# Optimization experiments

Measured on AMD Instinct MI355X. Metric: run time of the kernel, lower is better.

## Reference

```python
import jax, jax.numpy as jnp
import numpy as np

N = 50000
E = 1600000
IN, OUT = 128, 64


def _gcn(h, W, b, src, dst):
    # DGL GraphConv, norm='both', weight applied first (in>out), activation=relu
    x = h @ W  # [N, OUT]
    ones = jnp.ones((src.shape[0],), dtype=h.dtype)
    deg_out = jnp.clip(jax.ops.segment_sum(ones, src, num_segments=N), 1.0)
    deg_in = jnp.clip(jax.ops.segment_sum(ones, dst, num_segments=N), 1.0)
    x = x * jax.lax.rsqrt(deg_out)[:, None]
    agg = jax.ops.segment_sum(x[src], dst, num_segments=N)  # SpMM
    agg = agg * jax.lax.rsqrt(deg_in)[:, None]
    return jax.nn.relu(agg + b)


def setup_inputs() -> dict:
    key = jax.random.key(0)
    ks = jax.random.split(key, 10)
    inp = {"h": jax.random.normal(ks[0], (N, IN), dtype=jnp.float32)}
    for i in range(3):
        inp[f"src{i}"] = jax.random.randint(ks[1 + 2 * i], (E,), 0, N, dtype=jnp.int32)
        inp[f"dst{i}"] = jax.random.randint(ks[2 + 2 * i], (E,), 0, N, dtype=jnp.int32)
        inp[f"W{i}"] = jax.random.normal(ks[7 + i], (IN, OUT), dtype=jnp.float32) * (1.0 / np.sqrt(IN))
        inp[f"b{i}"] = jnp.zeros((OUT,), dtype=jnp.float32)
    return inp


def reference(h, src0, dst0, src1, dst1, src2, dst2, W0, b0, W1, b1, W2, b2):
    e0 = _gcn(h, W0, b0, src0, dst0)
    e1 = _gcn(h, W1, b1, src1, dst1)
    e2 = _gcn(h, W2, b2, src2, dst2)
    # stack over meta-path dim then mean == average of semantic embeddings
    return (e0 + e1 + e2) / 3.0
```

## Files before the change

kernel.cpp:

```cpp
#include <hip/hip_runtime.h>

#define KDIM 128
#define NCOLS 64
#define NHCH 64
#define HW 12500
#define BUCKET 64
#define NB7 782
#define FCAP 2816
#define NPB 85
#define PREP_HIST (3 * NHCH)
#define PREP_CNT  (3 * NPB)
#define PREP_WF   12
#define PREP_CONV 565
#define PREP_GRID (PREP_HIST + PREP_CNT + PREP_WF + PREP_CONV)

typedef __attribute__((ext_vector_type(8))) short bf16x8;
typedef __attribute__((ext_vector_type(4))) float f32x4;

struct GArgs {
  const int*   src[3];
  const int*   dst[3];
  const float* W[3];
  const float* b[3];
  int          E[3];
};

__device__ __forceinline__ unsigned short f2bf(float f) {
  unsigned u = __float_as_uint(f);
  u += 0x7FFFu + ((u >> 16) & 1u);
  return (unsigned short)(u >> 16);
}
__device__ __forceinline__ float bflo(unsigned u) { return __uint_as_float(u << 16); }
__device__ __forceinline__ float bfhi(unsigned u) { return __uint_as_float(u & 0xFFFF0000u); }

__global__ __launch_bounds__(256) void prep_kernel(
    GArgs A, const float* __restrict__ h, unsigned short* __restrict__ hb,
    unsigned short* __restrict__ Wf, unsigned* __restrict__ P8,
    int* __restrict__ tot, int total8) {
  __shared__ unsigned sbuf[HW];
  const int b = blockIdx.x;
  const int t = threadIdx.x;

  if (b < PREP_HIST) {
    const int g = b >> 6;
    const int chunk = b & 63;
    const int E = A.E[g];
    const int per_chunk = (((E + NHCH - 1) / NHCH) + 3) & ~3;
    const int* __restrict__ keys = A.src[g];
    for (int i = t; i < HW; i += 256) sbuf[i] = 0;
    __syncthreads();
    const int e0 = chunk * per_chunk;
    const int e1 = min(e0 + per_chunk, E);
    const int nn = max(e1 - e0, 0);
    const int nv = nn >> 2;
    const int4* k4p = (const int4*)&keys[e0];
    for (int v = t; v < nv; v += 256) {
      int4 k = k4p[v];
      atomicAdd(&sbuf[(unsigned)k.x >> 2], 1u << (((unsigned)k.x & 3u) * 8));
      atomicAdd(&sbuf[(unsigned)k.y >> 2], 1u << (((unsigned)k.y & 3u) * 8));
      atomicAdd(&sbuf[(unsigned)k.z >> 2], 1u << (((unsigned)k.z & 3u) * 8));
      atomicAdd(&sbuf[(unsigned)k.w >> 2], 1u << (((unsigned)k.w & 3u) * 8));
    }
    for (int e = e0 + (nv << 2) + t; e < e1; e += 256) {
      unsigned k = (unsigned)keys[e];
      atomicAdd(&sbuf[k >> 2], 1u << ((k & 3u) * 8));
    }
    __syncthreads();
    unsigned* __restrict__ dstp = P8 + (size_t)b * HW;
    for (int i = t; i < HW; i += 256) dstp[i] = sbuf[i];

  } else if (b < PREP_HIST + PREP_CNT) {
    const int bb = b - PREP_HIST;
    const int g = bb / NPB;
    const int blk = bb % NPB;
    const int E = A.E[g];
    const int per_block = (((E + NPB - 1) / NPB) + 3) & ~3;
    const int* __restrict__ dst = A.dst[g];
    int* hcnt = (int*)sbuf;
    for (int i = t; i < NB7; i += 256) hcnt[i] = 0;
    __syncthreads();
    const int e0 = blk * per_block;
    const int e1 = min(e0 + per_block, E);
    const int nn = max(e1 - e0, 0);
    const int nv = nn >> 2;
    const int4* d4 = (const int4*)&dst[e0];
    for (int v = t; v < nv; v += 256) {
      int4 d = d4[v];
      atomicAdd(&hcnt[(unsigned)d.x >> 6], 1);
      atomicAdd(&hcnt[(unsigned)d.y >> 6], 1);
      atomicAdd(&hcnt[(unsigned)d.z >> 6], 1);
      atomicAdd(&hcnt[(unsigned)d.w >> 6], 1);
    }
    for (int e = e0 + (nv << 2) + t; e < e1; e += 256)
      atomicAdd(&hcnt[(unsigned)dst[e] >> 6], 1);
    __syncthreads();
    for (int i = t; i < NB7; i += 256)
      if (hcnt[i]) atomicAdd(&tot[g * NB7 + i], hcnt[i]);

  } else if (b < PREP_HIST + PREP_CNT + PREP_WF) {
    int tid = (b - PREP_HIST - PREP_CNT) * 256 + t;
    int lane = tid & 63;
    int frag = (tid >> 6) & 15;
    int g = tid >> 10;
    int c = frag >> 2, kk = frag & 3;
    int n = lane & 15, quad = lane >> 4;
    const float* W = A.W[g];
    unsigned short v[8];
    #pragma unroll
    for (int j = 0; j < 8; ++j) {
      int k = 32 * kk + quad * 8 + j;
      v[j] = f2bf(W[k * 64 + 4 * n + c]);
    }
    uint4 u;
    u.x = (unsigned)v[0] | ((unsigned)v[1] << 16);
    u.y = (unsigned)v[2] | ((unsigned)v[3] << 16);
    u.z = (unsigned)v[4] | ((unsigned)v[5] << 16);
    u.w = (unsigned)v[6] | ((unsigned)v[7] << 16);
    ((uint4*)Wf)[tid] = u;

  } else {
    const int cb = b - (PREP_HIST + PREP_CNT + PREP_WF);
    for (int i = cb * 256 + t; i < total8; i += PREP_CONV * 256) {
      const float4* hp = (const float4*)(h + (size_t)i * 8);
      float4 f0 = hp[0];
      float4 f1 = hp[1];
      uint4 u;
      u.x = (unsigned)f2bf(f0.x) | ((unsigned)f2bf(f0.y) << 16);
      u.y = (unsigned)f2bf(f0.z) | ((unsigned)f2bf(f0.w) << 16);
      u.z = (unsigned)f2bf(f1.x) | ((unsigned)f2bf(f1.y) << 16);
      u.w = (unsigned)f2bf(f1.z) | ((unsigned)f2bf(f1.w) << 16);
      ((uint4*)hb)[i] = u;
    }
  }
}

__global__ __launch_bounds__(512) void scan782_kernel(
    const int* __restrict__ tot, int* __restrict__ off, int* __restrict__ cursor) {
  __shared__ int sd[512];
  const int g = blockIdx.x;
  const int t = threadIdx.x;
  int base = 0;
  for (int c0 = 0; c0 < NB7; c0 += 512) {
    int idx = c0 + t;
    int v = (idx < NB7) ? tot[g * NB7 + idx] : 0;
    sd[t] = v;
    __syncthreads();
    for (int o = 1; o < 512; o <<= 1) {
      int add = (t >= o) ? sd[t - o] : 0;
      __syncthreads();
      sd[t] += add;
      __syncthreads();
    }
    int excl = base + sd[t] - v;
    if (idx < NB7) {
      off[g * (NB7 + 1) + idx] = excl;
      cursor[g * NB7 + idx] = excl;
    }
    base += sd[511];
    __syncthreads();
  }
  if (t == 0) off[g * (NB7 + 1) + NB7] = base;
}

__global__ __launch_bounds__(256) void partition_fine_kernel(
    GArgs A, int* __restrict__ cursor, unsigned* __restrict__ P2, int Emax) {
  __shared__ int lcnt[NB7];
  __shared__ int lcur[NB7];
  const int g = blockIdx.y;
  const int E = A.E[g];
  const int per_block = (((E + NPB - 1) / NPB) + 3) & ~3;
  const int* __restrict__ src = A.src[g];
  const int* __restrict__ dst = A.dst[g];
  unsigned* __restrict__ P2g = P2 + (size_t)g * Emax;
  const int t = threadIdx.x;
  for (int i = t; i < NB7; i += 256) lcnt[i] = 0;
  __syncthreads();
  const int e0 = blockIdx.x * per_block;
  const int e1 = min(e0 + per_block, E);
  const int n = max(e1 - e0, 0);
  const int nv = n >> 2;
  const int4* d4 = (const int4*)&dst[e0];
  const int4* s4 = (const int4*)&src[e0];
  for (int v = t; v < nv; v += 256) {
    int4 d = d4[v];
    atomicAdd(&lcnt[(unsigned)d.x >> 6], 1);
    atomicAdd(&lcnt[(unsigned)d.y >> 6], 1);
    atomicAdd(&lcnt[(unsigned)d.z >> 6], 1);
    atomicAdd(&lcnt[(unsigned)d.w >> 6], 1);
  }
  for (int e = e0 + (nv << 2) + t; e < e1; e += 256)
    atomicAdd(&lcnt[(unsigned)dst[e] >> 6], 1);
  __syncthreads();
  for (int i = t; i < NB7; i += 256) {
    int c = lcnt[i];
    lcur[i] = c ? atomicAdd(&cursor[g * NB7 + i], c) : 0;
  }
  __syncthreads();
  for (int v = t; v < nv; v += 256) {
    int4 d = d4[v];
    int4 s = s4[v];
    unsigned bk; int pos;
    bk = (unsigned)d.x >> 6; pos = atomicAdd(&lcur[bk], 1);
    P2g[pos] = (unsigned)s.x | (((unsigned)d.x & 63u) << 16);
    bk = (unsigned)d.y >> 6; pos = atomicAdd(&lcur[bk], 1);
    P2g[pos] = (unsigned)s.y | (((unsigned)d.y & 63u) << 16);
    bk = (unsigned)d.z >> 6; pos = atomicAdd(&lcur[bk], 1);
    P2g[pos] = (unsigned)s.z | (((unsigned)d.z & 63u) << 16);
    bk = (unsigned)d.w >> 6; pos = atomicAdd(&lcur[bk], 1);
    P2g[pos] = (unsigned)s.w | (((unsigned)d.w & 63u) << 16);
  }
  for (int e = e0 + (nv << 2) + t; e < e1; e += 256) {
    unsigned d = (unsigned)dst[e];
    unsigned bk = d >> 6;
    int pos = atomicAdd(&lcur[bk], 1);
    P2g[pos] = (unsigned)src[e] | ((d & 63u) << 16);
  }
}

__global__ __launch_bounds__(512) void gemm_mfma_kernel(
    GArgs A, const unsigned short* __restrict__ hb,
    const unsigned short* __restrict__ Wf, const unsigned* __restrict__ P8,
    unsigned short* __restrict__ x, int N) {
  __shared__ unsigned ldegw[64];
  const int g = blockIdx.y;
  unsigned short* __restrict__ xg = x + (size_t)g * N * NCOLS;
  const int t = threadIdx.x;
  const int row0 = blockIdx.x * 128;

  if (t < 64) ldegw[t] = 0;
  __syncthreads();
  if (t < 256) {
    const unsigned* __restrict__ Pg = P8 + (size_t)g * NHCH * HW;
    const int widx = t >> 3;
    const int cg = t & 7;
    const int wcol = min((row0 >> 2) + widx, HW - 1);
    unsigned lo = 0, hi = 0;
    #pragma unroll
    for (int cc = 0; cc < 8; ++cc) {
      unsigned wv = Pg[(size_t)(cg * 8 + cc) * HW + wcol];
      lo += wv & 0x00FF00FFu;
      hi += (wv >> 8) & 0x00FF00FFu;
    }
    atomicAdd(&ldegw[2 * widx], lo);
    atomicAdd(&ldegw[2 * widx + 1], hi);
  }

  const int lane = t & 63;
  const int w = t >> 6;
  const int quad = lane >> 4;
  const int n = lane & 15;

  int arow = min(row0 + w * 16 + n, N - 1);
  const unsigned short* hrow = hb + (size_t)arow * KDIM + quad * 8;
  bf16x8 a0 = *(const bf16x8*)(hrow);
  bf16x8 a1 = *(const bf16x8*)(hrow + 32);
  bf16x8 a2 = *(const bf16x8*)(hrow + 64);
  bf16x8 a3 = *(const bf16x8*)(hrow + 96);

  const uint4* wfp = (const uint4*)Wf + (size_t)g * 1024 + lane;

  f32x4 acc[4];
  #pragma unroll
  for (int c = 0; c < 4; ++c) acc[c] = (f32x4)(0.f);

  __syncthreads();

  #pragma unroll
  for (int c = 0; c < 4; ++c) {
    union { uint4 u; bf16x8 v; } b0, b1, b2, b3;
    b0.u = wfp[(size_t)(c * 4 + 0) * 64];
    b1.u = wfp[(size_t)(c * 4 + 1) * 64];
    b2.u = wfp[(size_t)(c * 4 + 2) * 64];
    b3.u = wfp[(size_t)(c * 4 + 3) * 64];
    acc[c] = __builtin_amdgcn_mfma_f32_16x16x32_bf16(a0, b0.v, acc[c], 0, 0, 0);
    acc[c] = __builtin_amdgcn_mfma_f32_16x16x32_bf16(a1, b1.v, acc[c], 0, 0, 0);
    acc[c] = __builtin_amdgcn_mfma_f32_16x16x32_bf16(a2, b2.v, acc[c], 0, 0, 0);
    acc[c] = __builtin_amdgcn_mfma_f32_16x16x32_bf16(a3, b3.v, acc[c], 0, 0, 0);
  }

  const int rbase = row0 + w * 16 + quad * 4;
  #pragma unroll
  for (int r = 0; r < 4; ++r) {
    int row = rbase + r;
    if (row < N) {
      int lr = row - row0;
      float dg = (float)((ldegw[2 * (lr >> 2) + (lr & 1)] >> (((lr >> 1) & 1) * 16)) & 0xFFFFu);
      float s = rsqrtf(fmaxf(dg, 1.0f));
      uint2 o;
      o.x = (unsigned)f2bf(acc[0][r] * s) | ((unsigned)f2bf(acc[1][r] * s) << 16);
      o.y = (unsigned)f2bf(acc[2][r] * s) | ((unsigned)f2bf(acc[3][r] * s) << 16);
      *(uint2*)(xg + (size_t)row * NCOLS + 4 * n) = o;
    }
  }
}

__global__ __launch_bounds__(512) void spmm_all_kernel(
    GArgs A, const unsigned* __restrict__ P2, const int* __restrict__ off,
    const unsigned short* __restrict__ x, float* __restrict__ out,
    int N, int Emax) {
  __shared__ unsigned eb[FCAP];
  __shared__ unsigned short srcs[FCAP];
  __shared__ int cnt[BUCKET];
  __shared__ int cur[BUCKET];
  __shared__ int rsx[BUCKET + 1];

  const int t = threadIdx.x;
  const int bk = blockIdx.x;
  const int dbase = bk * BUCKET;
  const int nd = min(BUCKET, N - dbase);
  const int grp = t >> 3;
  const int qe = (t & 7) * 8;

  float tot[8];
  #pragma unroll
  for (int j = 0; j < 8; ++j) tot[j] = 0.f;

  for (int g = 0; g < 3; ++g) {
    const unsigned* __restrict__ P2g = P2 + (size_t)g * Emax;
    const unsigned short* __restrict__ xg = x + (size_t)g * N * NCOLS;

    __syncthreads();
    if (t < BUCKET) cnt[t] = 0;
    __syncthreads();

    const int e0 = off[g * (NB7 + 1) + bk];
    const int ne = min(off[g * (NB7 + 1) + bk + 1] - e0, FCAP);
    for (int i = t; i < ne; i += 512) {
      unsigned e = P2g[e0 + i];
      eb[i] = e;
      atomicAdd(&cnt[e >> 16], 1);
    }
    __syncthreads();

    if (t < BUCKET) {
      int v = cnt[t];
      int incl = v;
      #pragma unroll
      for (int o = 1; o < 64; o <<= 1) {
        int u = __shfl_up(incl, o, 64);
        if (t >= o) incl += u;
      }
      rsx[t + 1] = incl;
      cur[t] = incl - v;
      if (t == 0) rsx[0] = 0;
    }
    __syncthreads();

    for (int i = t; i < ne; i += 512) {
      unsigned e = eb[i];
      int pos = atomicAdd(&cur[e >> 16], 1);
      srcs[pos] = (unsigned short)(e & 0xFFFFu);
    }
    __syncthreads();

    if (grp < nd) {
      int i = rsx[grp];
      const int iend = rsx[grp + 1];
      const int deg = iend - i;
      float acc[8];
      #pragma unroll
      for (int j = 0; j < 8; ++j) acc[j] = 0.f;
      for (; i + 3 < iend; i += 4) {
        int sa = srcs[i + 0];
        int sb = srcs[i + 1];
        int sc = srcs[i + 2];
        int sdd = srcs[i + 3];
        uint4 ua = *(const uint4*)&xg[(size_t)sa * NCOLS + qe];
        uint4 ub = *(const uint4*)&xg[(size_t)sb * NCOLS + qe];
        uint4 uc = *(const uint4*)&xg[(size_t)sc * NCOLS + qe];
        uint4 ud = *(const uint4*)&xg[(size_t)sdd * NCOLS + qe];
        acc[0] += bflo(ua.x) + bflo(ub.x) + bflo(uc.x) + bflo(ud.x);
        acc[1] += bfhi(ua.x) + bfhi(ub.x) + bfhi(uc.x) + bfhi(ud.x);
        acc[2] += bflo(ua.y) + bflo(ub.y) + bflo(uc.y) + bflo(ud.y);
        acc[3] += bfhi(ua.y) + bfhi(ub.y) + bfhi(uc.y) + bfhi(ud.y);
        acc[4] += bflo(ua.z) + bflo(ub.z) + bflo(uc.z) + bflo(ud.z);
        acc[5] += bfhi(ua.z) + bfhi(ub.z) + bfhi(uc.z) + bfhi(ud.z);
        acc[6] += bflo(ua.w) + bflo(ub.w) + bflo(uc.w) + bflo(ud.w);
        acc[7] += bfhi(ua.w) + bfhi(ub.w) + bfhi(uc.w) + bfhi(ud.w);
      }
      for (; i < iend; ++i) {
        int s = srcs[i];
        uint4 u = *(const uint4*)&xg[(size_t)s * NCOLS + qe];
        acc[0] += bflo(u.x); acc[1] += bfhi(u.x);
        acc[2] += bflo(u.y); acc[3] += bfhi(u.y);
        acc[4] += bflo(u.z); acc[5] += bfhi(u.z);
        acc[6] += bflo(u.w); acc[7] += bfhi(u.w);
      }
      float sc2 = rsqrtf(fmaxf((float)deg, 1.0f));
      const float* bg = A.b[g] + qe;
      #pragma unroll
      for (int j = 0; j < 8; ++j)
        tot[j] += fmaxf(fmaf(acc[j], sc2, bg[j]), 0.f) * (1.0f / 3.0f);
    }
  }

  if (grp < nd) {
    float* op = &out[(size_t)(dbase + grp) * NCOLS + qe];
    *(float4*)&op[0] = make_float4(tot[0], tot[1], tot[2], tot[3]);
    *(float4*)&op[4] = make_float4(tot[4], tot[5], tot[6], tot[7]);
  }
}

extern "C" void kernel_launch(void* const* d_in, const int* in_sizes, int n_in,
                              void* d_out, int out_size, void* d_ws, size_t ws_size,
                              hipStream_t stream) {
  const float* h = (const float*)d_in[0];
  const int N = in_sizes[0] / KDIM;
  float* out = (float*)d_out;

  GArgs A;
  int Emax = 0;
  for (int g = 0; g < 3; ++g) {
    A.src[g] = (const int*)  d_in[1 + g * 4];
    A.dst[g] = (const int*)  d_in[2 + g * 4];
    A.W[g]   = (const float*)d_in[3 + g * 4];
    A.b[g]   = (const float*)d_in[4 + g * 4];
    A.E[g]   = in_sizes[1 + g * 4];
    if (A.E[g] > Emax) Emax = A.E[g];
  }

  char* w = (char*)d_ws;
  unsigned short* x = (unsigned short*)w;
  char* w2 = w + (size_t)3 * N * NCOLS * sizeof(unsigned short);
  unsigned short* hb = (unsigned short*)w2;
  char* w3 = w2 + (size_t)N * KDIM * sizeof(unsigned short);
  unsigned* P2 = (unsigned*)w3;
  char* w4 = w3 + (size_t)3 * Emax * sizeof(unsigned);
  unsigned* P8 = (unsigned*)w4;
  char* w5 = w4 + (size_t)3 * NHCH * HW * sizeof(unsigned);
  unsigned short* Wf = (unsigned short*)w5;
  char* w6 = w5 + (size_t)3 * 16 * 64 * 8 * sizeof(unsigned short);
  int* tot    = (int*)w6;
  int* cursor = tot + 3 * NB7;
  int* off    = cursor + 3 * NB7;

  hipMemsetAsync(tot, 0, 3 * NB7 * sizeof(int), stream);
  const int total8 = N * KDIM / 8;
  prep_kernel<<<PREP_GRID, 256, 0, stream>>>(A, h, hb, Wf, P8, tot, total8);
  scan782_kernel<<<3, 512, 0, stream>>>(tot, off, cursor);
  partition_fine_kernel<<<dim3(NPB, 3), 256, 0, stream>>>(A, cursor, P2, Emax);
  gemm_mfma_kernel<<<dim3((N + 127) / 128, 3), 512, 0, stream>>>(A, hb, Wf, P8, x, N);
  spmm_all_kernel<<<NB7, 512, 0, stream>>>(A, P2, off, x, out, N, Emax);
}
```

Before: 263.9 us.

## Fuse scan, partition and GEMM into one heterogeneous kernel launch

Merges the bucket-offset scan, the fine partition and the MFMA GEMM into a single kernel whose blocks split by index into partition blocks and GEMM blocks. Each partition block redundantly scans the bucket totals itself, with block 0 writing the offsets. Its cursor now starts at zero, is memset along with the totals, and only accumulates a relative offset on top of the scan. This removes two kernel launches and their dependency gaps and lets partitioning overlap with the GEMM. In exchange each partition block repeats the scan, partition blocks now use 512 threads, and the GEMM blocks carry the partition's larger shared-memory footprint, which may reduce occupancy.

```diff
diff --git a/kernel.cpp b/kernel.cpp
--- a/kernel.cpp
+++ b/kernel.cpp
@@ -13,6 +13,10 @@
 #define PREP_WF   12
 #define PREP_CONV 565
 #define PREP_GRID (PREP_HIST + PREP_CNT + PREP_WF + PREP_CONV)
+#define PG_PART (3 * NPB)
+#define PG_GEMM_PER 391
+#define PG_GEMM (3 * PG_GEMM_PER)
+#define PG_GRID (PG_PART + PG_GEMM)
 
 typedef __attribute__((ext_vector_type(8))) short bf16x8;
 typedef __attribute__((ext_vector_type(4))) float f32x4;
@@ -134,162 +138,166 @@
   }
 }
 
-__global__ __launch_bounds__(512) void scan782_kernel(
-    const int* __restrict__ tot, int* __restrict__ off, int* __restrict__ cursor) {
-  __shared__ int sd[512];
-  const int g = blockIdx.x;
-  const int t = threadIdx.x;
-  int base = 0;
-  for (int c0 = 0; c0 < NB7; c0 += 512) {
-    int idx = c0 + t;
-    int v = (idx < NB7) ? tot[g * NB7 + idx] : 0;
-    sd[t] = v;
-    __syncthreads();
-    for (int o = 1; o < 512; o <<= 1) {
-      int add = (t >= o) ? sd[t - o] : 0;
-      __syncthreads();
-      sd[t] += add;
-      __syncthreads();
-    }
-    int excl = base + sd[t] - v;
-    if (idx < NB7) {
-      off[g * (NB7 + 1) + idx] = excl;
-      cursor[g * NB7 + idx] = excl;
-    }
-    base += sd[511];
-    __syncthreads();
-  }
-  if (t == 0) off[g * (NB7 + 1) + NB7] = base;
-}
-
-__global__ __launch_bounds__(256) void partition_fine_kernel(
-    GArgs A, int* __restrict__ cursor, unsigned* __restrict__ P2, int Emax) {
+__global__ __launch_bounds__(512) void pg_kernel(
+    GArgs A, const unsigned short* __restrict__ hb,
+    const unsigned short* __restrict__ Wf, const unsigned* __restrict__ P8,
+    const int* __restrict__ tot, int* __restrict__ cursor,
+    int* __restrict__ off, unsigned* __restrict__ P2,
+    unsigned short* __restrict__ x, int N, int Emax) {
   __shared__ int lcnt[NB7];
   __shared__ int lcur[NB7];
-  const int g = blockIdx.y;
-  const int E = A.E[g];
-  const int per_block = (((E + NPB - 1) / NPB) + 3) & ~3;
-  const int* __restrict__ src = A.src[g];
-  const int* __restrict__ dst = A.dst[g];
-  unsigned* __restrict__ P2g = P2 + (size_t)g * Emax;
+  __shared__ int sd[512];
+  const int b = blockIdx.x;
   const int t = threadIdx.x;
-  for (int i = t; i < NB7; i += 256) lcnt[i] = 0;
-  __syncthreads();
-  const int e0 = blockIdx.x * per_block;
-  const int e1 = min(e0 + per_block, E);
-  const int n = max(e1 - e0, 0);
-  const int nv = n >> 2;
-  const int4* d4 = (const int4*)&dst[e0];
-  const int4* s4 = (const int4*)&src[e0];
-  for (int v = t; v < nv; v += 256) {
-    int4 d = d4[v];
-    atomicAdd(&lcnt[(unsigned)d.x >> 6], 1);
-    atomicAdd(&lcnt[(unsigned)d.y >> 6], 1);
-    atomicAdd(&lcnt[(unsigned)d.z >> 6], 1);
-    atomicAdd(&lcnt[(unsigned)d.w >> 6], 1);
-  }
-  for (int e = e0 + (nv << 2) + t; e < e1; e += 256)
-    atomicAdd(&lcnt[(unsigned)dst[e] >> 6], 1);
-  __syncthreads();
-  for (int i = t; i < NB7; i += 256) {
-    int c = lcnt[i];
-    lcur[i] = c ? atomicAdd(&cursor[g * NB7 + i], c) : 0;
-  }
-  __syncthreads();
-  for (int v = t; v < nv; v += 256) {
-    int4 d = d4[v];
-    int4 s = s4[v];
-    unsigned bk; int pos;
-    bk = (unsigned)d.x >> 6; pos = atomicAdd(&lcur[bk], 1);
-    P2g[pos] = (unsigned)s.x | (((unsigned)d.x & 63u) << 16);
-    bk = (unsigned)d.y >> 6; pos = atomicAdd(&lcur[bk], 1);
-    P2g[pos] = (unsigned)s.y | (((unsigned)d.y & 63u) << 16);
-    bk = (unsigned)d.z >> 6; pos = atomicAdd(&lcur[bk], 1);
-    P2g[pos] = (unsigned)s.z | (((unsigned)d.z & 63u) << 16);
-    bk = (unsigned)d.w >> 6; pos = atomicAdd(&lcur[bk], 1);
-    P2g[pos] = (unsigned)s.w | (((unsigned)d.w & 63u) << 16);
-  }
-  for (int e = e0 + (nv << 2) + t; e < e1; e += 256) {
-    unsigned d = (unsigned)dst[e];
-    unsigned bk = d >> 6;
-    int pos = atomicAdd(&lcur[bk], 1);
-    P2g[pos] = (unsigned)src[e] | ((d & 63u) << 16);
-  }
-}
-
-__global__ __launch_bounds__(512) void gemm_mfma_kernel(
-    GArgs A, const unsigned short* __restrict__ hb,
-    const unsigned short* __restrict__ Wf, const unsigned* __restrict__ P8,
-    unsigned short* __restrict__ x, int N) {
-  __shared__ unsigned ldegw[64];
-  const int g = blockIdx.y;
-  unsigned short* __restrict__ xg = x + (size_t)g * N * NCOLS;
-  const int t = threadIdx.x;
-  const int row0 = blockIdx.x * 128;
-
-  if (t < 64) ldegw[t] = 0;
-  __syncthreads();
-  if (t < 256) {
-    const unsigned* __restrict__ Pg = P8 + (size_t)g * NHCH * HW;
-    const int widx = t >> 3;
-    const int cg = t & 7;
-    const int wcol = min((row0 >> 2) + widx, HW - 1);
-    unsigned lo = 0, hi = 0;
+
+  if (b < PG_PART) {
+    const int g = b / NPB;
+    const int blk = b % NPB;
+    const int E = A.E[g];
+    const int per_block = (((E + NPB - 1) / NPB) + 3) & ~3;
+    const int* __restrict__ src = A.src[g];
+    const int* __restrict__ dst = A.dst[g];
+    unsigned* __restrict__ P2g = P2 + (size_t)g * Emax;
+
+    for (int i = t; i < NB7; i += 512) lcnt[i] = 0;
+    __syncthreads();
+    const int e0 = blk * per_block;
+    const int e1 = min(e0 + per_block, E);
+    const int nn = max(e1 - e0, 0);
+    const int nv = nn >> 2;
+    const int4* d4 = (const int4*)&dst[e0];
+    const int4* s4 = (const int4*)&src[e0];
+    for (int v = t; v < nv; v += 512) {
+      int4 d = d4[v];
+      atomicAdd(&lcnt[(unsigned)d.x >> 6], 1);
+      atomicAdd(&lcnt[(unsigned)d.y >> 6], 1);
+      atomicAdd(&lcnt[(unsigned)d.z >> 6], 1);
+      atomicAdd(&lcnt[(unsigned)d.w >> 6], 1);
+    }
+    for (int e = e0 + (nv << 2) + t; e < e1; e += 512)
+      atomicAdd(&lcnt[(unsigned)dst[e] >> 6], 1);
+    __syncthreads();
+
+    int base = 0;
+    for (int c0 = 0; c0 < NB7; c0 += 512) {
+      int idx = c0 + t;
+      int v = (idx < NB7) ? tot[g * NB7 + idx] : 0;
+      sd[t] = v;
+      __syncthreads();
+      for (int o = 1; o < 512; o <<= 1) {
+        int add = (t >= o) ? sd[t - o] : 0;
+        __syncthreads();
+        sd[t] += add;
+        __syncthreads();
+      }
+      int excl = base + sd[t] - v;
+      if (idx < NB7) {
+        lcur[idx] = excl;
+        if (blk == 0) off[g * (NB7 + 1) + idx] = excl;
+      }
+      base += sd[511];
+      __syncthreads();
+    }
+    if (blk == 0 && t == 0) off[g * (NB7 + 1) + NB7] = base;
+
+    for (int i = t; i < NB7; i += 512) {
+      int c = lcnt[i];
+      if (c) lcur[i] += atomicAdd(&cursor[g * NB7 + i], c);
+    }
+    __syncthreads();
+
+    for (int v = t; v < nv; v += 512) {
+      int4 d = d4[v];
+      int4 s = s4[v];
+      unsigned bk; int pos;
+      bk = (unsigned)d.x >> 6; pos = atomicAdd(&lcur[bk], 1);
+      P2g[pos] = (unsigned)s.x | (((unsigned)d.x & 63u) << 16);
+      bk = (unsigned)d.y >> 6; pos = atomicAdd(&lcur[bk], 1);
+      P2g[pos] = (unsigned)s.y | (((unsigned)d.y & 63u) << 16);
+      bk = (unsigned)d.z >> 6; pos = atomicAdd(&lcur[bk], 1);
+      P2g[pos] = (unsigned)s.z | (((unsigned)d.z & 63u) << 16);
+      bk = (unsigned)d.w >> 6; pos = atomicAdd(&lcur[bk], 1);
+      P2g[pos] = (unsigned)s.w | (((unsigned)d.w & 63u) << 16);
+    }
+    for (int e = e0 + (nv << 2) + t; e < e1; e += 512) {
+      unsigned d = (unsigned)dst[e];
+      unsigned bk = d >> 6;
+      int pos = atomicAdd(&lcur[bk], 1);
+      P2g[pos] = (unsigned)src[e] | ((d & 63u) << 16);
+    }
+
+  } else {
+    unsigned* ldegw = (unsigned*)lcnt;
+    const int gb = b - PG_PART;
+    const int g = gb / PG_GEMM_PER;
+    const int blk = gb % PG_GEMM_PER;
+    const int row0 = blk * 128;
+    unsigned short* __restrict__ xg = x + (size_t)g * N * NCOLS;
+
+    if (t < 64) ldegw[t] = 0;
+    __syncthreads();
+    if (t < 256) {
+      const unsigned* __restrict__ Pg = P8 + (size_t)g * NHCH * HW;
+      const int widx = t >> 3;
+      const int cg = t & 7;
+      const int wcol = min((row0 >> 2) + widx, HW - 1);
+      unsigned lo = 0, hi = 0;
+      #pragma unroll
+      for (int cc = 0; cc < 8; ++cc) {
+        unsigned wv = Pg[(size_t)(cg * 8 + cc) * HW + wcol];
+        lo += wv & 0x00FF00FFu;
+        hi += (wv >> 8) & 0x00FF00FFu;
+      }
+      atomicAdd(&ldegw[2 * widx], lo);
+      atomicAdd(&ldegw[2 * widx + 1], hi);
+    }
+
+    const int lane = t & 63;
+    const int w = t >> 6;
+    const int quad = lane >> 4;
+    const int n = lane & 15;
+
+    int arow = min(row0 + w * 16 + n, N - 1);
+    const unsigned short* hrow = hb + (size_t)arow * KDIM + quad * 8;
+    bf16x8 a0 = *(const bf16x8*)(hrow);
+    bf16x8 a1 = *(const bf16x8*)(hrow + 32);
+    bf16x8 a2 = *(const bf16x8*)(hrow + 64);
+    bf16x8 a3 = *(const bf16x8*)(hrow + 96);
+
+    const uint4* wfp = (const uint4*)Wf + (size_t)g * 1024 + lane;
+
+    f32x4 acc[4];
     #pragma unroll
-    for (int cc = 0; cc < 8; ++cc) {
-      unsigned wv = Pg[(size_t)(cg * 8 + cc) * HW + wcol];
-      lo += wv & 0x00FF00FFu;
-      hi += (wv >> 8) & 0x00FF00FFu;
-    }
-    atomicAdd(&ldegw[2 * widx], lo);
-    atomicAdd(&ldegw[2 * widx + 1], hi);
-  }
-
-  const int lane = t & 63;
-  const int w = t >> 6;
-  const int quad = lane >> 4;
-  const int n = lane & 15;
-
-  int arow = min(row0 + w * 16 + n, N - 1);
-  const unsigned short* hrow = hb + (size_t)arow * KDIM + quad * 8;
-  bf16x8 a0 = *(const bf16x8*)(hrow);
-  bf16x8 a1 = *(const bf16x8*)(hrow + 32);
-  bf16x8 a2 = *(const bf16x8*)(hrow + 64);
-  bf16x8 a3 = *(const bf16x8*)(hrow + 96);
-
-  const uint4* wfp = (const uint4*)Wf + (size_t)g * 1024 + lane;
-
-  f32x4 acc[4];
-  #pragma unroll
-  for (int c = 0; c < 4; ++c) acc[c] = (f32x4)(0.f);
-
-  __syncthreads();
-
-  #pragma unroll
-  for (int c = 0; c < 4; ++c) {
-    union { uint4 u; bf16x8 v; } b0, b1, b2, b3;
-    b0.u = wfp[(size_t)(c * 4 + 0) * 64];
-    b1.u = wfp[(size_t)(c * 4 + 1) * 64];
-    b2.u = wfp[(size_t)(c * 4 + 2) * 64];
-    b3.u = wfp[(size_t)(c * 4 + 3) * 64];
-    acc[c] = __builtin_amdgcn_mfma_f32_16x16x32_bf16(a0, b0.v, acc[c], 0, 0, 0);
-    acc[c] = __builtin_amdgcn_mfma_f32_16x16x32_bf16(a1, b1.v, acc[c], 0, 0, 0);
-    acc[c] = __builtin_amdgcn_mfma_f32_16x16x32_bf16(a2, b2.v, acc[c], 0, 0, 0);
-    acc[c] = __builtin_amdgcn_mfma_f32_16x16x32_bf16(a3, b3.v, acc[c], 0, 0, 0);
-  }
-
-  const int rbase = row0 + w * 16 + quad * 4;
-  #pragma unroll
-  for (int r = 0; r < 4; ++r) {
-    int row = rbase + r;
-    if (row < N) {
-      int lr = row - row0;
-      float dg = (float)((ldegw[2 * (lr >> 2) + (lr & 1)] >> (((lr >> 1) & 1) * 16)) & 0xFFFFu);
-      float s = rsqrtf(fmaxf(dg, 1.0f));
-      uint2 o;
-      o.x = (unsigned)f2bf(acc[0][r] * s) | ((unsigned)f2bf(acc[1][r] * s) << 16);
-      o.y = (unsigned)f2bf(acc[2][r] * s) | ((unsigned)f2bf(acc[3][r] * s) << 16);
-      *(uint2*)(xg + (size_t)row * NCOLS + 4 * n) = o;
+    for (int c = 0; c < 4; ++c) acc[c] = (f32x4)(0.f);
+
+    __syncthreads();
+
+    #pragma unroll
+    for (int c = 0; c < 4; ++c) {
+      union { uint4 u; bf16x8 v; } b0, b1, b2, b3;
+      b0.u = wfp[(size_t)(c * 4 + 0) * 64];
+      b1.u = wfp[(size_t)(c * 4 + 1) * 64];
+      b2.u = wfp[(size_t)(c * 4 + 2) * 64];
+      b3.u = wfp[(size_t)(c * 4 + 3) * 64];
+      acc[c] = __builtin_amdgcn_mfma_f32_16x16x32_bf16(a0, b0.v, acc[c], 0, 0, 0);
+      acc[c] = __builtin_amdgcn_mfma_f32_16x16x32_bf16(a1, b1.v, acc[c], 0, 0, 0);
+      acc[c] = __builtin_amdgcn_mfma_f32_16x16x32_bf16(a2, b2.v, acc[c], 0, 0, 0);
+      acc[c] = __builtin_amdgcn_mfma_f32_16x16x32_bf16(a3, b3.v, acc[c], 0, 0, 0);
+    }
+
+    const int rbase = row0 + w * 16 + quad * 4;
+    #pragma unroll
+    for (int r = 0; r < 4; ++r) {
+      int row = rbase + r;
+      if (row < N) {
+        int lr = row - row0;
+        float dg = (float)((ldegw[2 * (lr >> 2) + (lr & 1)] >> (((lr >> 1) & 1) * 16)) & 0xFFFFu);
+        float s = rsqrtf(fmaxf(dg, 1.0f));
+        uint2 o;
+        o.x = (unsigned)f2bf(acc[0][r] * s) | ((unsigned)f2bf(acc[1][r] * s) << 16);
+        o.y = (unsigned)f2bf(acc[2][r] * s) | ((unsigned)f2bf(acc[3][r] * s) << 16);
+        *(uint2*)(xg + (size_t)row * NCOLS + 4 * n) = o;
+      }
     }
   }
 }
@@ -434,11 +442,9 @@
   int* cursor = tot + 3 * NB7;
   int* off    = cursor + 3 * NB7;
 
-  hipMemsetAsync(tot, 0, 3 * NB7 * sizeof(int), stream);
+  hipMemsetAsync(tot, 0, 2 * 3 * NB7 * sizeof(int), stream);
   const int total8 = N * KDIM / 8;
   prep_kernel<<<PREP_GRID, 256, 0, stream>>>(A, h, hb, Wf, P8, tot, total8);
-  scan782_kernel<<<3, 512, 0, stream>>>(tot, off, cursor);
-  partition_fine_kernel<<<dim3(NPB, 3), 256, 0, stream>>>(A, cursor, P2, Emax);
-  gemm_mfma_kernel<<<dim3((N + 127) / 128, 3), 512, 0, stream>>>(A, hb, Wf, P8, x, N);
+  pg_kernel<<<PG_GRID, 512, 0, stream>>>(A, hb, Wf, P8, tot, cursor, off, P2, x, N, Emax);
   spmm_all_kernel<<<NB7, 512, 0, stream>>>(A, P2, off, x, out, N, Emax);
 }
```

Result: faster. 251.8 us (-4.6%).
